# Optimization experiments

Measured on AMD Instinct MI355X. Metric: run time of the kernel, lower is better.

Reference implementation:

```python
import jax, jax.numpy as jnp
import numpy as np

B, Q, D = 4, 8192, 256
H, L, P = 8, 4, 4
HD = D // H
SPATIAL = [(128, 128), (64, 64), (32, 32), (16, 16)]


def setup_inputs() -> dict:
    key = jax.random.key(0)
    ks = jax.random.split(key, 12)
    inp = {
        "query": jax.random.normal(ks[0], (B, Q, D), jnp.float32),
        "feat0": jax.random.normal(ks[1], (B, D) + SPATIAL[0], jnp.float32),
        "feat1": jax.random.normal(ks[2], (B, D) + SPATIAL[1], jnp.float32),
        "feat2": jax.random.normal(ks[3], (B, D) + SPATIAL[2], jnp.float32),
        "feat3": jax.random.normal(ks[4], (B, D) + SPATIAL[3], jnp.float32),
        "reference_points": jax.random.uniform(ks[5], (B, Q, 2), jnp.float32),
        "W_off": jax.random.normal(ks[6], (D, H * L * P * 2), jnp.float32) * 0.02,
        "b_off": jnp.zeros((H * L * P * 2,), jnp.float32),
        "W_attn": jax.random.normal(ks[7], (D, H * L * P), jnp.float32) * 0.02,
        "b_attn": jnp.zeros((H * L * P,), jnp.float32),
        "W_out": jax.random.normal(ks[8], (D, D), jnp.float32) * 0.02,
        "b_out": jnp.zeros((D,), jnp.float32),
    }
    return inp


def _bilinear_sample(img, grid):
    # img: (C, Hf, Wf); grid: (N, 2) with (x, y) in [-1, 1]; align_corners=True,
    # padding_mode='zeros' semantics (out-of-range corners contribute 0).
    C, Hf, Wf = img.shape
    x = (grid[:, 0] + 1.0) * 0.5 * (Wf - 1)
    y = (grid[:, 1] + 1.0) * 0.5 * (Hf - 1)
    x0 = jnp.floor(x)
    y0 = jnp.floor(y)
    x1 = x0 + 1.0
    y1 = y0 + 1.0
    wx1 = x - x0
    wx0 = 1.0 - wx1
    wy1 = y - y0
    wy0 = 1.0 - wy1

    def gather(xi, yi):
        valid = (xi >= 0) & (xi <= Wf - 1) & (yi >= 0) & (yi <= Hf - 1)
        xc = jnp.clip(xi, 0, Wf - 1).astype(jnp.int32)
        yc = jnp.clip(yi, 0, Hf - 1).astype(jnp.int32)
        return img[:, yc, xc] * valid.astype(img.dtype)  # (C, N)

    out = (gather(x0, y0) * (wx0 * wy0)
           + gather(x1, y0) * (wx1 * wy0)
           + gather(x0, y1) * (wx0 * wy1)
           + gather(x1, y1) * (wx1 * wy1))
    return out  # (C, N)


_sample_bh = jax.vmap(_bilinear_sample)  # over fused (B*H) axis


def _msdeform(query, feats, reference_points,
              W_off, b_off, W_attn, b_attn, W_out, b_out):
    offsets = jnp.tanh(query @ W_off + b_off).reshape(B, Q, H, L, P, 2)
    logits = (query @ W_attn + b_attn).reshape(B, Q, H, L * P)
    attn = jax.nn.softmax(logits, axis=3).reshape(B, Q, H, L, P)
    ref_grid = reference_points * 2.0 - 1.0  # (B, Q, 2)

    agg = jnp.zeros((B, Q, H, HD), dtype=query.dtype)
    for lvl, feat in enumerate(feats):
        Hf, Wf = feat.shape[2], feat.shape[3]
        img = feat.reshape(B * H, HD, Hf, Wf)
        # (B, H, Q, P, 2)
        grid = ref_grid[:, None, :, None, :] + jnp.transpose(
            offsets[:, :, :, lvl], (0, 2, 1, 3, 4))
        grid = grid.reshape(B * H, Q * P, 2)
        samp = _sample_bh(img, grid).reshape(B, H, HD, Q, P)
        agg = agg + jnp.einsum('bhcqp,bqhp->bqhc', samp, attn[:, :, :, lvl, :])

    out = agg.reshape(B, Q, D) @ W_out + b_out
    return out, attn


def reference(query, feat0, feat1, feat2, feat3, reference_points,
              W_off, b_off, W_attn, b_attn, W_out, b_out):
    return _msdeform(query, [feat0, feat1, feat2, feat3], reference_points,
                     W_off, b_off, W_attn, b_attn, W_out, b_out)
```

## Files before the change

### kernel.cpp

```cpp
#include <hip/hip_runtime.h>
#include <cstdint>
#include <cstddef>

#define NB 4
#define NQ 8192
#define ND 256
#define NH 8
#define NL 4
#define NP 4
#define QBLK 16

__global__ __launch_bounds__(256) void transpose_k(
    const float* __restrict__ in, float* __restrict__ out, int HW) {
  __shared__ float tile[32][33];
  int yx0 = blockIdx.x << 5;
  int d0  = blockIdx.y << 5;
  int b   = blockIdx.z;
  const float* inb = in + (size_t)b * ND * HW;
  float* outb = out + (size_t)b * HW * ND;
  int col = threadIdx.x & 31;
  int row = threadIdx.x >> 5;
#pragma unroll
  for (int r = 0; r < 4; ++r) {
    int d = row + (r << 3);
    tile[d][col] = inb[(size_t)(d0 + d) * HW + (yx0 + col)];
  }
  __syncthreads();
#pragma unroll
  for (int r = 0; r < 4; ++r) {
    int y = row + (r << 3);
    outb[(size_t)(yx0 + y) * ND + (d0 + col)] = tile[col][y];
  }
}

__global__ __launch_bounds__(192) void proj_k(
    const float* __restrict__ query, const float* __restrict__ refp,
    const float* __restrict__ W_off, const float* __restrict__ b_off,
    const float* __restrict__ W_attn, const float* __restrict__ b_attn,
    float* __restrict__ pos, float* __restrict__ attn_out) {
  int q0 = blockIdx.x * QBLK;
  __shared__ float qs[QBLK][ND];
  __shared__ float lg[QBLK][128];
  int t = threadIdx.x;
  {
    const float4* qsrc = (const float4*)(query + (size_t)q0 * ND);
    float4* qdst = (float4*)&qs[0][0];
#pragma unroll
    for (int i = 0; i < 6; ++i) {
      int idx = t + 192 * i;
      if (idx < QBLK * ND / 4) qdst[idx] = qsrc[idx];
    }
  }
  __syncthreads();
  if (t < 128) {
    int slot = t & 63, qg = t >> 6;
    int j0 = slot << 2;
    float4 bb = *(const float4*)(b_off + j0);
    float4 acc[8];
#pragma unroll
    for (int qq = 0; qq < 8; ++qq) acc[qq] = bb;
    const float* qbase = &qs[qg * 8][0];
#pragma unroll 4
    for (int k = 0; k < ND; ++k) {
      float4 w = *(const float4*)(W_off + (size_t)k * 256 + j0);
#pragma unroll
      for (int qq = 0; qq < 8; ++qq) {
        float qk = qbase[qq * ND + k];
        acc[qq].x = fmaf(qk, w.x, acc[qq].x);
        acc[qq].y = fmaf(qk, w.y, acc[qq].y);
        acc[qq].z = fmaf(qk, w.z, acc[qq].z);
        acc[qq].w = fmaf(qk, w.w, acc[qq].w);
      }
    }
#pragma unroll
    for (int qq = 0; qq < 8; ++qq) {
      int bq = q0 + qg * 8 + qq;
      float rx = refp[bq * 2 + 0] * 2.f - 1.f;
      float ry = refp[bq * 2 + 1] * 2.f - 1.f;
      float4 r;
      r.x = rx + tanhf(acc[qq].x);
      r.y = ry + tanhf(acc[qq].y);
      r.z = rx + tanhf(acc[qq].z);
      r.w = ry + tanhf(acc[qq].w);
      *(float4*)(pos + (size_t)bq * 256 + j0) = r;
    }
  } else {
    int u = t - 128;
    int slot = u & 31, qg = u >> 5;
    int j0 = slot << 2;
    float4 bb = *(const float4*)(b_attn + j0);
    float4 acc[8];
#pragma unroll
    for (int qq = 0; qq < 8; ++qq) acc[qq] = bb;
    const float* qbase = &qs[qg * 8][0];
#pragma unroll 4
    for (int k = 0; k < ND; ++k) {
      float4 w = *(const float4*)(W_attn + (size_t)k * 128 + j0);
#pragma unroll
      for (int qq = 0; qq < 8; ++qq) {
        float qk = qbase[qq * ND + k];
        acc[qq].x = fmaf(qk, w.x, acc[qq].x);
        acc[qq].y = fmaf(qk, w.y, acc[qq].y);
        acc[qq].z = fmaf(qk, w.z, acc[qq].z);
        acc[qq].w = fmaf(qk, w.w, acc[qq].w);
      }
    }
#pragma unroll
    for (int qq = 0; qq < 8; ++qq) {
      int qi = qg * 8 + qq;
      lg[qi][j0 + 0] = acc[qq].x;
      lg[qi][j0 + 1] = acc[qq].y;
      lg[qi][j0 + 2] = acc[qq].z;
      lg[qi][j0 + 3] = acc[qq].w;
    }
  }
  __syncthreads();
  if (t < 128) {
    int qi = t >> 3;
    int h = t & 7;
    float* l = &lg[qi][h * 16];
    float m = -1e30f;
#pragma unroll
    for (int i = 0; i < 16; ++i) m = fmaxf(m, l[i]);
    float e[16], s = 0.f;
#pragma unroll
    for (int i = 0; i < 16; ++i) { e[i] = __expf(l[i] - m); s += e[i]; }
    float inv = 1.f / s;
#pragma unroll
    for (int i = 0; i < 16; ++i) l[i] = e[i] * inv;
  }
  __syncthreads();
  {
    const float4* src = (const float4*)&lg[0][0];
    float4* dst = (float4*)(attn_out + (size_t)q0 * 128);
#pragma unroll
    for (int i = 0; i < 3; ++i) {
      int idx = t + 192 * i;
      if (idx < QBLK * 128 / 4) dst[idx] = src[idx];
    }
  }
}

__global__ __launch_bounds__(256) void sample_k(
    const float* __restrict__ fT0, const float* __restrict__ fT1,
    const float* __restrict__ fT2, const float* __restrict__ fT3,
    const float* __restrict__ pos, const float* __restrict__ attnw,
    float* __restrict__ agg) {
  int bq = blockIdx.x;
  int b = bq >> 13;
  __shared__ float ps[256];
  __shared__ float as[128];
  int t = threadIdx.x;
  ps[t] = pos[(size_t)bq * 256 + t];
  if (t < 128) as[t] = attnw[(size_t)bq * 128 + t];
  __syncthreads();
  int h = t >> 5;
  int c = t & 31;
  int d = (h << 5) + c;
  const float* fts[4] = {
      fT0 + (size_t)b * 16384 * ND, fT1 + (size_t)b * 4096 * ND,
      fT2 + (size_t)b * 1024 * ND, fT3 + (size_t)b * 256 * ND};
  const int HFs[4] = {128, 64, 32, 16};
  const int WFs[4] = {128, 64, 32, 16};
  float acc = 0.f;
#pragma unroll
  for (int l = 0; l < 4; ++l) {
    const float* ft = fts[l];
    const int Hf = HFs[l], Wf = WFs[l];
#pragma unroll
    for (int p = 0; p < 4; ++p) {
      int idx = ((h * 4 + l) * 4 + p);
      float gx = ps[idx * 2 + 0];
      float gy = ps[idx * 2 + 1];
      float a = as[idx];
      float x = (gx + 1.f) * 0.5f * (float)(Wf - 1);
      float y = (gy + 1.f) * 0.5f * (float)(Hf - 1);
      float x0f = floorf(x), y0f = floorf(y);
      float wx1 = x - x0f, wx0 = 1.f - wx1;
      float wy1 = y - y0f, wy0 = 1.f - wy1;
      int x0 = (int)x0f, y0 = (int)y0f;
      int x1 = x0 + 1, y1 = y0 + 1;
      bool vx0 = (x0 >= 0) && (x0 <= Wf - 1);
      bool vx1 = (x1 >= 0) && (x1 <= Wf - 1);
      bool vy0 = (y0 >= 0) && (y0 <= Hf - 1);
      bool vy1 = (y1 >= 0) && (y1 <= Hf - 1);
      int xc0 = min(max(x0, 0), Wf - 1), xc1 = min(max(x1, 0), Wf - 1);
      int yc0 = min(max(y0, 0), Hf - 1), yc1 = min(max(y1, 0), Hf - 1);
      float v00 = ft[((size_t)(yc0 * Wf + xc0)) * ND + d];
      float v10 = ft[((size_t)(yc0 * Wf + xc1)) * ND + d];
      float v01 = ft[((size_t)(yc1 * Wf + xc0)) * ND + d];
      float v11 = ft[((size_t)(yc1 * Wf + xc1)) * ND + d];
      float w00 = (vx0 && vy0) ? wx0 * wy0 : 0.f;
      float w10 = (vx1 && vy0) ? wx1 * wy0 : 0.f;
      float w01 = (vx0 && vy1) ? wx0 * wy1 : 0.f;
      float w11 = (vx1 && vy1) ? wx1 * wy1 : 0.f;
      float s = v00 * w00 + v10 * w10 + v01 * w01 + v11 * w11;
      acc = fmaf(a, s, acc);
    }
  }
  agg[(size_t)bq * 256 + d] = acc;
}

__global__ __launch_bounds__(128) void out_k(
    const float* __restrict__ agg, const float* __restrict__ W_out,
    const float* __restrict__ b_out, float* __restrict__ out) {
  int q0 = blockIdx.x * QBLK;
  __shared__ float as_[QBLK][ND];
  int t = threadIdx.x;
  {
    const float4* src = (const float4*)(agg + (size_t)q0 * ND);
    float4* dst = (float4*)&as_[0][0];
#pragma unroll
    for (int i = 0; i < 8; ++i) dst[t + 128 * i] = src[t + 128 * i];
  }
  __syncthreads();
  int slot = t & 63, qg = t >> 6;
  int j0 = slot << 2;
  float4 bb = *(const float4*)(b_out + j0);
  float4 acc[8];
#pragma unroll
  for (int qq = 0; qq < 8; ++qq) acc[qq] = bb;
  const float* abase = &as_[qg * 8][0];
#pragma unroll 4
  for (int k = 0; k < ND; ++k) {
    float4 w = *(const float4*)(W_out + (size_t)k * 256 + j0);
#pragma unroll
    for (int qq = 0; qq < 8; ++qq) {
      float ak = abase[qq * ND + k];
      acc[qq].x = fmaf(ak, w.x, acc[qq].x);
      acc[qq].y = fmaf(ak, w.y, acc[qq].y);
      acc[qq].z = fmaf(ak, w.z, acc[qq].z);
      acc[qq].w = fmaf(ak, w.w, acc[qq].w);
    }
  }
#pragma unroll
  for (int qq = 0; qq < 8; ++qq) {
    *(float4*)(out + (size_t)(q0 + qg * 8 + qq) * 256 + j0) = acc[qq];
  }
}

extern "C" void kernel_launch(void* const* d_in, const int* in_sizes, int n_in,
                              void* d_out, int out_size, void* d_ws,
                              size_t ws_size, hipStream_t stream) {
  const float* query  = (const float*)d_in[0];
  const float* feat0  = (const float*)d_in[1];
  const float* feat1  = (const float*)d_in[2];
  const float* feat2  = (const float*)d_in[3];
  const float* feat3  = (const float*)d_in[4];
  const float* refp   = (const float*)d_in[5];
  const float* W_off  = (const float*)d_in[6];
  const float* b_off  = (const float*)d_in[7];
  const float* W_attn = (const float*)d_in[8];
  const float* b_attn = (const float*)d_in[9];
  const float* W_out  = (const float*)d_in[10];
  const float* b_out  = (const float*)d_in[11];

  float* out = (float*)d_out;
  float* attn_out = out + (size_t)NB * NQ * ND;

  float* ws  = (float*)d_ws;
  float* fT0 = ws;
  float* fT1 = fT0 + (size_t)NB * 16384 * ND;
  float* fT2 = fT1 + (size_t)NB * 4096 * ND;
  float* fT3 = fT2 + (size_t)NB * 1024 * ND;
  float* pos = fT3 + (size_t)NB * 256 * ND;
  float* agg = pos + (size_t)NB * NQ * ND;

  transpose_k<<<dim3(512, 8, NB), 256, 0, stream>>>(feat0, fT0, 16384);
  transpose_k<<<dim3(128, 8, NB), 256, 0, stream>>>(feat1, fT1, 4096);
  transpose_k<<<dim3(32, 8, NB), 256, 0, stream>>>(feat2, fT2, 1024);
  transpose_k<<<dim3(8, 8, NB), 256, 0, stream>>>(feat3, fT3, 256);

  proj_k<<<dim3(NB * NQ / QBLK), 192, 0, stream>>>(query, refp, W_off, b_off,
                                                   W_attn, b_attn, pos,
                                                   attn_out);
  sample_k<<<dim3(NB * NQ), 256, 0, stream>>>(fT0, fT1, fT2, fT3, pos,
                                              attn_out, agg);
  out_k<<<dim3(NB * NQ / QBLK), 128, 0, stream>>>(agg, W_out, b_out, out);
}
```

Before: 498.3 us.

## Precompute bilinear corner table in LDS and gather float4 channels per thread

The sampling kernel now processes four queries per block. It first builds a shared-memory table of corner offsets and attention-scaled bilinear weights, which removes the per-thread redundant coordinate math. Each thread then gathers float4 channel vectors instead of scalar floats, so it issues fewer load instructions. Block IDs are swizzled across batch/query chunks to spread work and improve cache locality. Offsets use 32-bit ints into a single workspace base, which assumes the workspace fits in the int range.

```diff
diff --git a/kernel.cpp b/kernel.cpp
--- a/kernel.cpp
+++ b/kernel.cpp
@@ -141,64 +141,84 @@
   }
 }
 
+#define HPAD 136
 __global__ __launch_bounds__(256) void sample_k(
-    const float* __restrict__ fT0, const float* __restrict__ fT1,
-    const float* __restrict__ fT2, const float* __restrict__ fT3,
-    const float* __restrict__ pos, const float* __restrict__ attnw,
-    float* __restrict__ agg) {
-  int bq = blockIdx.x;
-  int b = bq >> 13;
-  __shared__ float ps[256];
-  __shared__ float as[128];
+    const float* __restrict__ feat_ws, const float* __restrict__ pos,
+    const float* __restrict__ attnw, float* __restrict__ agg) {
+  __shared__ int tbl[4 * NH * HPAD];
+  int bid = blockIdx.x;
+  int wk = ((bid & 7) << 10) | (bid >> 3);
+  int q0 = wk << 2;
+  int b = wk >> 11;
   int t = threadIdx.x;
-  ps[t] = pos[(size_t)bq * 256 + t];
-  if (t < 128) as[t] = attnw[(size_t)bq * 128 + t];
-  __syncthreads();
-  int h = t >> 5;
-  int c = t & 31;
-  int d = (h << 5) + c;
-  const float* fts[4] = {
-      fT0 + (size_t)b * 16384 * ND, fT1 + (size_t)b * 4096 * ND,
-      fT2 + (size_t)b * 1024 * ND, fT3 + (size_t)b * 256 * ND};
-  const int HFs[4] = {128, 64, 32, 16};
-  const int WFs[4] = {128, 64, 32, 16};
-  float acc = 0.f;
-#pragma unroll
-  for (int l = 0; l < 4; ++l) {
-    const float* ft = fts[l];
-    const int Hf = HFs[l], Wf = WFs[l];
-#pragma unroll
-    for (int p = 0; p < 4; ++p) {
-      int idx = ((h * 4 + l) * 4 + p);
-      float gx = ps[idx * 2 + 0];
-      float gy = ps[idx * 2 + 1];
-      float a = as[idx];
-      float x = (gx + 1.f) * 0.5f * (float)(Wf - 1);
-      float y = (gy + 1.f) * 0.5f * (float)(Hf - 1);
-      float x0f = floorf(x), y0f = floorf(y);
-      float wx1 = x - x0f, wx0 = 1.f - wx1;
-      float wy1 = y - y0f, wy0 = 1.f - wy1;
-      int x0 = (int)x0f, y0 = (int)y0f;
-      int x1 = x0 + 1, y1 = y0 + 1;
-      bool vx0 = (x0 >= 0) && (x0 <= Wf - 1);
-      bool vx1 = (x1 >= 0) && (x1 <= Wf - 1);
-      bool vy0 = (y0 >= 0) && (y0 <= Hf - 1);
-      bool vy1 = (y1 >= 0) && (y1 <= Hf - 1);
-      int xc0 = min(max(x0, 0), Wf - 1), xc1 = min(max(x1, 0), Wf - 1);
-      int yc0 = min(max(y0, 0), Hf - 1), yc1 = min(max(y1, 0), Hf - 1);
-      float v00 = ft[((size_t)(yc0 * Wf + xc0)) * ND + d];
-      float v10 = ft[((size_t)(yc0 * Wf + xc1)) * ND + d];
-      float v01 = ft[((size_t)(yc1 * Wf + xc0)) * ND + d];
-      float v11 = ft[((size_t)(yc1 * Wf + xc1)) * ND + d];
-      float w00 = (vx0 && vy0) ? wx0 * wy0 : 0.f;
-      float w10 = (vx1 && vy0) ? wx1 * wy0 : 0.f;
-      float w01 = (vx0 && vy1) ? wx0 * wy1 : 0.f;
-      float w11 = (vx1 && vy1) ? wx1 * wy1 : 0.f;
-      float s = v00 * w00 + v10 * w10 + v01 * w01 + v11 * w11;
-      acc = fmaf(a, s, acc);
-    }
-  }
-  agg[(size_t)bq * 256 + d] = acc;
+
+  const int FT1 = NB * 16384 * ND;
+  const int FT2 = FT1 + NB * 4096 * ND;
+  const int FT3 = FT2 + NB * 1024 * ND;
+  int lb[4] = {b * 16384 * ND, FT1 + b * 4096 * ND, FT2 + b * 1024 * ND,
+               FT3 + b * 256 * ND};
+
+#pragma unroll
+  for (int j = t; j < 512; j += 256) {
+    int qi = j >> 7, i = j & 127;
+    int bq = q0 + qi;
+    float gx = pos[(size_t)bq * 256 + 2 * i];
+    float gy = pos[(size_t)bq * 256 + 2 * i + 1];
+    float a = attnw[(size_t)bq * 128 + i];
+    int l = (i >> 2) & 3;
+    int Wf = 128 >> l;
+    float wf1 = (float)(Wf - 1);
+    float x = (gx + 1.f) * 0.5f * wf1;
+    float y = (gy + 1.f) * 0.5f * wf1;
+    float x0f = floorf(x), y0f = floorf(y);
+    float wx1 = x - x0f, wx0 = 1.f - wx1;
+    float wy1 = y - y0f, wy0 = 1.f - wy1;
+    int x0 = (int)x0f, y0 = (int)y0f;
+    int x1 = x0 + 1, y1 = y0 + 1;
+    bool vx0 = (x0 >= 0) && (x0 < Wf);
+    bool vx1 = (x1 >= 0) && (x1 < Wf);
+    bool vy0 = (y0 >= 0) && (y0 < Wf);
+    bool vy1 = (y1 >= 0) && (y1 < Wf);
+    int xc0 = min(max(x0, 0), Wf - 1), xc1 = min(max(x1, 0), Wf - 1);
+    int yc0 = min(max(y0, 0), Wf - 1), yc1 = min(max(y1, 0), Wf - 1);
+    int base = lb[l];
+    int o00 = base + (yc0 * Wf + xc0) * ND;
+    int o10 = base + (yc0 * Wf + xc1) * ND;
+    int o01 = base + (yc1 * Wf + xc0) * ND;
+    int o11 = base + (yc1 * Wf + xc1) * ND;
+    float w00 = (vx0 && vy0) ? a * wx0 * wy0 : 0.f;
+    float w10 = (vx1 && vy0) ? a * wx1 * wy0 : 0.f;
+    float w01 = (vx0 && vy1) ? a * wx0 * wy1 : 0.f;
+    float w11 = (vx1 && vy1) ? a * wx1 * wy1 : 0.f;
+    int h = i >> 4, s = i & 15;
+    int* rec = &tbl[(qi * NH + h) * HPAD + s * 8];
+    rec[0] = o00; rec[1] = __float_as_int(w00);
+    rec[2] = o10; rec[3] = __float_as_int(w10);
+    rec[4] = o01; rec[5] = __float_as_int(w01);
+    rec[6] = o11; rec[7] = __float_as_int(w11);
+  }
+  __syncthreads();
+
+  int lane = t & 63, qi = t >> 6;
+  int h = lane >> 3, cq = lane & 7;
+  int bq = q0 + qi;
+  int choff = (h << 5) + (cq << 2);
+  const int* rec = &tbl[(qi * NH + h) * HPAD];
+  float4 acc = {0.f, 0.f, 0.f, 0.f};
+#pragma unroll 4
+  for (int s = 0; s < 16; ++s) {
+#pragma unroll
+    for (int c = 0; c < 4; ++c) {
+      int off = rec[s * 8 + c * 2];
+      float w = __int_as_float(rec[s * 8 + c * 2 + 1]);
+      float4 v = *(const float4*)(feat_ws + off + choff);
+      acc.x = fmaf(w, v.x, acc.x);
+      acc.y = fmaf(w, v.y, acc.y);
+      acc.z = fmaf(w, v.z, acc.z);
+      acc.w = fmaf(w, v.w, acc.w);
+    }
+  }
+  *(float4*)(agg + (size_t)bq * 256 + choff) = acc;
 }
 
 __global__ __launch_bounds__(128) void out_k(
@@ -274,7 +294,6 @@
   proj_k<<<dim3(NB * NQ / QBLK), 192, 0, stream>>>(query, refp, W_off, b_off,
                                                    W_attn, b_attn, pos,
                                                    attn_out);
-  sample_k<<<dim3(NB * NQ), 256, 0, stream>>>(fT0, fT1, fT2, fT3, pos,
-                                              attn_out, agg);
+  sample_k<<<dim3(NB * NQ / 4), 256, 0, stream>>>(fT0, pos, attn_out, agg);
   out_k<<<dim3(NB * NQ / QBLK), 128, 0, stream>>>(agg, W_out, b_out, out);
 }
```

Result: faster. 467.0 us (-6.3%).
